# Performance work log

Measured on AMD Instinct MI355X. Metric: run time of the kernel, lower is better.

The kernel has to match this reference:

```python
import jax, jax.numpy as jnp
import numpy as np

OFF_THRESH = 0.5  # stand-in for specials.OFF_THRESH


def _smap3x3(x_value, y_value, z_value, r_mask, key_query):
    B, C = x_value.shape[0], x_value.shape[1]
    H, W = x_value.shape[-2], x_value.shape[-1]
    dt = x_value.dtype

    z_values = z_value.reshape(B, C, 1, H, W)
    r_m = r_mask.reshape(B, C, 1, H, W)
    x_z = jnp.concatenate([x_value, y_value, z_value], axis=2)  # [B,C,3,H,W]

    # argmin over the 3x3 window dim -> one-hot selection mask [B,C,9,H,W]
    ind = jnp.argmin(key_query, axis=2)                      # [B,C,H,W]
    w = jnp.moveaxis(jax.nn.one_hot(ind, 9, dtype=dt), -1, 2)  # [B,C,9,H,W]

    valid = (r_m > OFF_THRESH) & (z_values > 0.0)            # [B,C,1,H,W]
    w = jnp.where(valid, w, jnp.zeros((), dt))

    center = jnp.zeros((9,), dt).at[4].set(1.0).reshape(1, 1, 9, 1, 1)
    bad = (r_m > OFF_THRESH) & ~(z_values > 0.0)
    # torch.where(1 - bad > 0.5, w, temp) == where(bad, center, w)
    w = jnp.where(bad, center, w)

    wd = jax.lax.stop_gradient(w).reshape(B, C, 3, 3, H, W)
    # outer product over window (s,t) and xyz (z) dims -> [B,C,3,3,3,H,W]
    new_xz = jnp.einsum('bcsthw,bczhw->bcstzhw', wd, x_z)

    w2 = jnp.where(valid, w, center)
    new_r = (jax.lax.stop_gradient(w2) * r_m).reshape(B, C, 3, 3, 1, H, W)

    return jnp.concatenate([new_xz, new_r], axis=4)  # [B,C,3,3,4,H,W]


def setup_inputs() -> dict:
    key = jax.random.key(0)
    k1, k2, k3, k4, k5 = jax.random.split(key, 5)
    B, C, H, W = 4, 1, 480, 640
    return {
        "x_value": jax.random.normal(k1, (B, C, 1, H, W), dtype=jnp.float32),
        "y_value": jax.random.normal(k2, (B, C, 1, H, W), dtype=jnp.float32),
        "z_value": jax.random.normal(k3, (B, C, 1, H, W), dtype=jnp.float32),
        "r_mask": jax.random.uniform(k4, (B, C, 1, H, W), dtype=jnp.float32),
        "key_query": jax.random.normal(k5, (B, C, 9, H, W), dtype=jnp.float32),
    }


def reference(x_value, y_value, z_value, r_mask, key_query):
    return _smap3x3(x_value, y_value, z_value, r_mask, key_query)
```

## Files before the change

kernel.cpp:

```cpp
#include <hip/hip_runtime.h>


constexpr int H = 480;
constexpr int W = 640;
constexpr int HW = H * W;
constexpr int HW4 = HW / 4;
constexpr int BLK = 256;
constexpr int GRIDX = HW4 / BLK;

typedef __attribute__((ext_vector_type(4))) float fvec4;

__device__ __forceinline__ fvec4 nt_load4(const fvec4* p) {
    return __builtin_nontemporal_load(p);
}
__device__ __forceinline__ void nt_store4(fvec4* p, fvec4 v) {
    __builtin_nontemporal_store(v, p);
}

__global__ __launch_bounds__(256) void smap3x3_kernel(
    const fvec4* __restrict__ x,
    const fvec4* __restrict__ y,
    const fvec4* __restrict__ z,
    const fvec4* __restrict__ r,
    const fvec4* __restrict__ kq,
    fvec4* __restrict__ out)
{
    const int hw4 = blockIdx.x * BLK + threadIdx.x;
    const int b   = blockIdx.y;
    const size_t pix = (size_t)b * HW4 + hw4;

    const fvec4 xv = nt_load4(x + pix);
    const fvec4 yv = nt_load4(y + pix);
    const fvec4 zv = nt_load4(z + pix);
    const fvec4 rv = nt_load4(r + pix);

    const fvec4* kqb = kq + (size_t)b * 9 * HW4 + hw4;
    fvec4 best = nt_load4(kqb);
    int i0 = 0, i1 = 0, i2 = 0, i3 = 0;
#pragma unroll
    for (int k = 1; k < 9; ++k) {
        const fvec4 kk = nt_load4(kqb + (size_t)k * HW4);
        if (kk.x < best.x) { best.x = kk.x; i0 = k; }
        if (kk.y < best.y) { best.y = kk.y; i1 = k; }
        if (kk.z < best.z) { best.z = kk.z; i2 = k; }
        if (kk.w < best.w) { best.w = kk.w; i3 = k; }
    }

    int sw0, sw1, sw2, sw3;
    int s20, s21, s22, s23;
    { const bool ron = rv.x > 0.5f, zon = zv.x > 0.0f;
      sw0 = ron ? (zon ? i0 : 4) : -1;  s20 = (ron && zon) ? i0 : 4; }
    { const bool ron = rv.y > 0.5f, zon = zv.y > 0.0f;
      sw1 = ron ? (zon ? i1 : 4) : -1;  s21 = (ron && zon) ? i1 : 4; }
    { const bool ron = rv.z > 0.5f, zon = zv.z > 0.0f;
      sw2 = ron ? (zon ? i2 : 4) : -1;  s22 = (ron && zon) ? i2 : 4; }
    { const bool ron = rv.w > 0.5f, zon = zv.w > 0.0f;
      sw3 = ron ? (zon ? i3 : 4) : -1;  s23 = (ron && zon) ? i3 : 4; }

    fvec4* outb = out + (size_t)b * 36 * HW4 + hw4;
#pragma unroll
    for (int k = 0; k < 9; ++k) {
        fvec4 ox, oy, oz, orr;
        const bool m0 = (k == sw0), m1 = (k == sw1), m2 = (k == sw2), m3 = (k == sw3);
        ox.x = m0 ? xv.x : 0.0f;  ox.y = m1 ? xv.y : 0.0f;
        ox.z = m2 ? xv.z : 0.0f;  ox.w = m3 ? xv.w : 0.0f;
        oy.x = m0 ? yv.x : 0.0f;  oy.y = m1 ? yv.y : 0.0f;
        oy.z = m2 ? yv.z : 0.0f;  oy.w = m3 ? yv.w : 0.0f;
        oz.x = m0 ? zv.x : 0.0f;  oz.y = m1 ? zv.y : 0.0f;
        oz.z = m2 ? zv.z : 0.0f;  oz.w = m3 ? zv.w : 0.0f;
        orr.x = (k == s20) ? rv.x : 0.0f;  orr.y = (k == s21) ? rv.y : 0.0f;
        orr.z = (k == s22) ? rv.z : 0.0f;  orr.w = (k == s23) ? rv.w : 0.0f;

        nt_store4(outb + (size_t)(4 * k + 0) * HW4, ox);
        nt_store4(outb + (size_t)(4 * k + 1) * HW4, oy);
        nt_store4(outb + (size_t)(4 * k + 2) * HW4, oz);
        nt_store4(outb + (size_t)(4 * k + 3) * HW4, orr);
    }
}

extern "C" void kernel_launch(void* const* d_in, const int* in_sizes, int n_in,
                              void* d_out, int out_size, void* d_ws, size_t ws_size,
                              hipStream_t stream) {
    const fvec4* x  = (const fvec4*)d_in[0];
    const fvec4* y  = (const fvec4*)d_in[1];
    const fvec4* z  = (const fvec4*)d_in[2];
    const fvec4* r  = (const fvec4*)d_in[3];
    const fvec4* kq = (const fvec4*)d_in[4];
    fvec4* out = (fvec4*)d_out;

    dim3 grid(GRIDX, 4);
    smap3x3_kernel<<<grid, dim3(BLK), 0, stream>>>(x, y, z, r, kq, out);
}
```

Baseline: 225.6 us.

## Split into selection kernel and per-plane contiguous write kernel

```diff
diff --git a/kernel.cpp b/kernel.cpp
--- a/kernel.cpp
+++ b/kernel.cpp
@@ -5,8 +5,12 @@
 constexpr int W = 640;
 constexpr int HW = H * W;
 constexpr int HW4 = HW / 4;
+constexpr int B = 4;
 constexpr int BLK = 256;
-constexpr int GRIDX = HW4 / BLK;
+constexpr int GRIDX1 = HW4 / BLK;
+constexpr int S2 = 50;
+constexpr int CHUNK4 = HW4 / S2;
+constexpr int ITERS2 = CHUNK4 / BLK;
 
 typedef __attribute__((ext_vector_type(4))) float fvec4;
 
@@ -17,22 +21,18 @@
     __builtin_nontemporal_store(v, p);
 }
 
-__global__ __launch_bounds__(256) void smap3x3_kernel(
-    const fvec4* __restrict__ x,
-    const fvec4* __restrict__ y,
+__global__ __launch_bounds__(256) void smap_sel_kernel(
     const fvec4* __restrict__ z,
     const fvec4* __restrict__ r,
     const fvec4* __restrict__ kq,
-    fvec4* __restrict__ out)
+    unsigned int* __restrict__ sel)
 {
     const int hw4 = blockIdx.x * BLK + threadIdx.x;
     const int b   = blockIdx.y;
     const size_t pix = (size_t)b * HW4 + hw4;
 
-    const fvec4 xv = nt_load4(x + pix);
-    const fvec4 yv = nt_load4(y + pix);
-    const fvec4 zv = nt_load4(z + pix);
-    const fvec4 rv = nt_load4(r + pix);
+    const fvec4 zv = z[pix];
+    const fvec4 rv = r[pix];
 
     const fvec4* kqb = kq + (size_t)b * 9 * HW4 + hw4;
     fvec4 best = nt_load4(kqb);
@@ -46,35 +46,60 @@
         if (kk.w < best.w) { best.w = kk.w; i3 = k; }
     }
 
-    int sw0, sw1, sw2, sw3;
-    int s20, s21, s22, s23;
+    unsigned int b0, b1, b2, b3;
     { const bool ron = rv.x > 0.5f, zon = zv.x > 0.0f;
-      sw0 = ron ? (zon ? i0 : 4) : -1;  s20 = (ron && zon) ? i0 : 4; }
+      const int sw = ron ? (zon ? i0 : 4) : -1;
+      const int s2 = (ron && zon) ? i0 : 4;
+      b0 = (unsigned)((sw + 1) << 4) | (unsigned)s2; }
     { const bool ron = rv.y > 0.5f, zon = zv.y > 0.0f;
-      sw1 = ron ? (zon ? i1 : 4) : -1;  s21 = (ron && zon) ? i1 : 4; }
+      const int sw = ron ? (zon ? i1 : 4) : -1;
+      const int s2 = (ron && zon) ? i1 : 4;
+      b1 = (unsigned)((sw + 1) << 4) | (unsigned)s2; }
     { const bool ron = rv.z > 0.5f, zon = zv.z > 0.0f;
-      sw2 = ron ? (zon ? i2 : 4) : -1;  s22 = (ron && zon) ? i2 : 4; }
+      const int sw = ron ? (zon ? i2 : 4) : -1;
+      const int s2 = (ron && zon) ? i2 : 4;
+      b2 = (unsigned)((sw + 1) << 4) | (unsigned)s2; }
     { const bool ron = rv.w > 0.5f, zon = zv.w > 0.0f;
-      sw3 = ron ? (zon ? i3 : 4) : -1;  s23 = (ron && zon) ? i3 : 4; }
+      const int sw = ron ? (zon ? i3 : 4) : -1;
+      const int s2 = (ron && zon) ? i3 : 4;
+      b3 = (unsigned)((sw + 1) << 4) | (unsigned)s2; }
 
-    fvec4* outb = out + (size_t)b * 36 * HW4 + hw4;
+    sel[pix] = b0 | (b1 << 8) | (b2 << 16) | (b3 << 24);
+}
+
+__global__ __launch_bounds__(256) void smap_write_kernel(
+    const fvec4* __restrict__ x,
+    const fvec4* __restrict__ y,
+    const fvec4* __restrict__ z,
+    const fvec4* __restrict__ r,
+    const unsigned int* __restrict__ sel,
+    fvec4* __restrict__ out)
+{
+    const int kc = blockIdx.y;
+    const int k  = kc >> 2;
+    const int c  = kc & 3;
+    const int bb = blockIdx.z;
+
+    const fvec4* vp = (c == 0) ? x : (c == 1) ? y : (c == 2) ? z : r;
+    vp += (size_t)bb * HW4;
+    const unsigned int* sp = sel + (size_t)bb * HW4;
+    fvec4* op = out + ((size_t)bb * 36 + kc) * HW4;
+
+    const int base = blockIdx.x * CHUNK4;
+    const unsigned int tgt = (c < 3) ? (unsigned)(k + 1) : (unsigned)k;
+    const int shift = (c < 3) ? 4 : 0;
+
 #pragma unroll
-    for (int k = 0; k < 9; ++k) {
-        fvec4 ox, oy, oz, orr;
-        const bool m0 = (k == sw0), m1 = (k == sw1), m2 = (k == sw2), m3 = (k == sw3);
-        ox.x = m0 ? xv.x : 0.0f;  ox.y = m1 ? xv.y : 0.0f;
-        ox.z = m2 ? xv.z : 0.0f;  ox.w = m3 ? xv.w : 0.0f;
-        oy.x = m0 ? yv.x : 0.0f;  oy.y = m1 ? yv.y : 0.0f;
-        oy.z = m2 ? yv.z : 0.0f;  oy.w = m3 ? yv.w : 0.0f;
-        oz.x = m0 ? zv.x : 0.0f;  oz.y = m1 ? zv.y : 0.0f;
-        oz.z = m2 ? zv.z : 0.0f;  oz.w = m3 ? zv.w : 0.0f;
-        orr.x = (k == s20) ? rv.x : 0.0f;  orr.y = (k == s21) ? rv.y : 0.0f;
-        orr.z = (k == s22) ? rv.z : 0.0f;  orr.w = (k == s23) ? rv.w : 0.0f;
-
-        nt_store4(outb + (size_t)(4 * k + 0) * HW4, ox);
-        nt_store4(outb + (size_t)(4 * k + 1) * HW4, oy);
-        nt_store4(outb + (size_t)(4 * k + 2) * HW4, oz);
-        nt_store4(outb + (size_t)(4 * k + 3) * HW4, orr);
+    for (int it = 0; it < ITERS2; ++it) {
+        const int f = base + it * BLK + threadIdx.x;
+        const unsigned int s = sp[f];
+        const fvec4 v = vp[f];
+        fvec4 o;
+        o.x = (((s >> (shift))      & 15u) == tgt) ? v.x : 0.0f;
+        o.y = (((s >> (shift + 8))  & 15u) == tgt) ? v.y : 0.0f;
+        o.z = (((s >> (shift + 16)) & 15u) == tgt) ? v.z : 0.0f;
+        o.w = (((s >> (shift + 24)) & 15u) == tgt) ? v.w : 0.0f;
+        nt_store4(op + f, o);
     }
 }
 
@@ -87,7 +112,8 @@
     const fvec4* r  = (const fvec4*)d_in[3];
     const fvec4* kq = (const fvec4*)d_in[4];
     fvec4* out = (fvec4*)d_out;
+    unsigned int* sel = (unsigned int*)d_ws;
 
-    dim3 grid(GRIDX, 4);
-    smap3x3_kernel<<<grid, dim3(BLK), 0, stream>>>(x, y, z, r, kq, out);
+    smap_sel_kernel<<<dim3(GRIDX1, B), dim3(BLK), 0, stream>>>(z, r, kq, sel);
+    smap_write_kernel<<<dim3(S2, 36, B), dim3(BLK), 0, stream>>>(x, y, z, r, sel, out);
 }
```

Result: slower. 241.0 us (+6.8%).
